# Kernel optimization log

Hardware: AMD Instinct MI355X
Metric: run time of the kernel (lower is better)

Reference implementation:

```python
import jax, jax.numpy as jnp
import numpy as np

N = 50000        # nodes
E = 800000       # edges (no self-loops; loops added in reference per PyG GATConv default)
IN = 128         # in_channels
OUT = 32         # out_channels
HEADS = 4
HID = HEADS * OUT  # 128
NEG_SLOPE = 0.2
BN_EPS = 1e-5
INV_SQRT2 = 0.7071067811865476


def setup_inputs() -> dict:
    key = jax.random.key(0)
    ks = jax.random.split(key, 20)
    x = jax.random.normal(ks[0], (N, IN), dtype=jnp.float32)
    src = jax.random.randint(ks[1], (E,), 0, N)
    dst = jax.random.randint(ks[2], (E,), 0, N)
    dst = jnp.where(src == dst, (dst + 1) % N, dst)  # no self-loops in base graph
    edge_index = jnp.stack([src, dst], axis=0)
    def lin(k, fan_in, shape):
        return jax.random.normal(k, shape, dtype=jnp.float32) / np.float32(np.sqrt(fan_in))
    return {
        "x": x,
        "edge_index": edge_index,
        "W1": lin(ks[3], IN, (IN, HID)),
        "att_src1": 0.1 * jax.random.normal(ks[4], (HEADS, OUT), dtype=jnp.float32),
        "att_dst1": 0.1 * jax.random.normal(ks[5], (HEADS, OUT), dtype=jnp.float32),
        "bias1": jnp.zeros((HID,), jnp.float32),
        "W2": lin(ks[6], HID, (HID, HID)),
        "att_src2": 0.1 * jax.random.normal(ks[7], (1, HID), dtype=jnp.float32),
        "att_dst2": 0.1 * jax.random.normal(ks[8], (1, HID), dtype=jnp.float32),
        "bias2": jnp.zeros((HID,), jnp.float32),
        "gamma1": jnp.ones((HID,), jnp.float32),
        "beta1": jnp.zeros((HID,), jnp.float32),
        "gamma2": jnp.ones((HID,), jnp.float32),
        "beta2": jnp.zeros((HID,), jnp.float32),
        "W_res": lin(ks[9], IN, (IN, HID)),
        "b_res": jnp.zeros((HID,), jnp.float32),
        "W_fin": lin(ks[10], HID, (HID, OUT)),
        "b_fin": jnp.zeros((OUT,), jnp.float32),
    }


def gat_conv(x, src, dst, W, a_src, a_dst, bias, heads, out_ch):
    h = (x @ W).reshape(-1, heads, out_ch)                    # [N, H, C]
    alpha_s = jnp.sum(h * a_src, axis=-1)                      # [N, H]
    alpha_d = jnp.sum(h * a_dst, axis=-1)                      # [N, H]
    e = jax.nn.leaky_relu(alpha_s[src] + alpha_d[dst], NEG_SLOPE)  # [E, H]
    # segment softmax over incoming edges of each destination node
    m = jax.ops.segment_max(e, dst, num_segments=N)
    e = jnp.exp(e - m[dst])
    denom = jax.ops.segment_sum(e, dst, num_segments=N)
    alpha = e / (denom[dst] + 1e-16)                           # [E, H]
    msg = h[src] * alpha[..., None]                            # [E, H, C]
    out = jax.ops.segment_sum(msg, dst, num_segments=N)        # [N, H, C]
    return out.reshape(-1, heads * out_ch) + bias


def batch_norm(h, gamma, beta):
    mu = h.mean(axis=0)
    var = jnp.mean((h - mu) ** 2, axis=0)  # biased, as torch BN training forward
    return (h - mu) * jax.lax.rsqrt(var + BN_EPS) * gamma + beta


def reference(x, edge_index, W1, att_src1, att_dst1, bias1, W2, att_src2, att_dst2,
              bias2, gamma1, beta1, gamma2, beta2, W_res, b_res, W_fin, b_fin):
    loops = jnp.arange(N, dtype=edge_index.dtype)
    src = jnp.concatenate([edge_index[0], loops])
    dst = jnp.concatenate([edge_index[1], loops])
    h = gat_conv(x, src, dst, W1, att_src1, att_dst1, bias1, HEADS, OUT)
    h = jax.nn.relu(batch_norm(h, gamma1, beta1))
    h = gat_conv(h, src, dst, W2, att_src2, att_dst2, bias2, 1, HID)
    h = jax.nn.relu(batch_norm(h, gamma2, beta2))
    residual = x @ W_res + b_res
    return ((h + residual) * INV_SQRT2) @ W_fin + b_fin        # [N, OUT]
```

## Files before the change

### kernel.cpp

```cpp
#include <hip/hip_runtime.h>
#include <hip/hip_fp16.h>
#include <type_traits>

#define NEG_SLOPE 0.2f
#define INV_SQRT2 0.7071067811865476f
#define BCAP 8192

typedef _Float16 half8 __attribute__((ext_vector_type(8)));
typedef float floatx4 __attribute__((ext_vector_type(4)));

__device__ __forceinline__ float lrelu(float x) { return x > 0.f ? x : NEG_SLOPE * x; }


__global__ __launch_bounds__(256) void prep_weights(const float* __restrict__ W1,
                                                    const float* __restrict__ W2,
                                                    const float* __restrict__ Wres,
                                                    const float* __restrict__ Wfin,
                                                    _Float16* __restrict__ W1t,
                                                    _Float16* __restrict__ W2t,
                                                    _Float16* __restrict__ Wrt,
                                                    _Float16* __restrict__ Wft,
                                                    int* __restrict__ bfill) {
    if (blockIdx.x == 0) bfill[threadIdx.x] = 0;
    int i = blockIdx.x * 256 + threadIdx.x;
    if (i < 16384) {
        int k = i >> 7, n = i & 127;
        W1t[n * 136 + k] = (_Float16)W1[i];
    } else if (i < 32768) {
        int j = i - 16384; int k = j >> 7, n = j & 127;
        W2t[n * 136 + k] = (_Float16)W2[j];
    } else if (i < 49152) {
        int j = i - 32768; int k = j >> 7, n = j & 127;
        Wrt[n * 136 + k] = (_Float16)Wres[j];
    } else if (i < 53248) {
        int j = i - 49152; int k = j >> 5, n = j & 31;
        Wft[n * 136 + k] = (_Float16)Wfin[j];
    }
}


__global__ __launch_bounds__(256) void bucket_scatter(const int* __restrict__ src,
                                                      const int* __restrict__ dst,
                                                      int* __restrict__ bucket_fill,
                                                      unsigned* __restrict__ staging,
                                                      int E, int N, int chunk) {
    __shared__ int lds[256];
    int tid = threadIdx.x;
    int M = E + N;
    int begin = blockIdx.x * chunk;
    int endc = min(begin + chunk, M);
    lds[tid] = 0;
    __syncthreads();
    for (int i = begin + tid; i < endc; i += 256) {
        int d = (i < E) ? dst[i] : (i - E);
        atomicAdd(&lds[d >> 8], 1);
    }
    __syncthreads();
    int h = lds[tid];
    int base = 0;
    if (h > 0) base = atomicAdd(&bucket_fill[tid], h);
    __syncthreads();
    lds[tid] = base;
    __syncthreads();
    for (int i = begin + tid; i < endc; i += 256) {
        int s, d;
        if (i < E) { s = src[i]; d = dst[i]; } else { s = d = i - E; }
        int b = d >> 8;
        int r = atomicAdd(&lds[b], 1);
        if (r < BCAP) staging[b * BCAP + r] = (unsigned)s | ((unsigned)(d & 255) << 24);
    }
}

__global__ __launch_bounds__(256) void fine_sort(const unsigned* __restrict__ staging,
                                                 const int* __restrict__ bucket_fill,
                                                 int* __restrict__ row_ptr,
                                                 int* __restrict__ csr_src, int NB, int N) {
    __shared__ int sb[256];
    __shared__ int c1[256];
    __shared__ int s1[256];
    int t = threadIdx.x;
    int b = blockIdx.x;
    int c = (t < NB) ? min(bucket_fill[t], BCAP) : 0;
    sb[t] = c;
    __syncthreads();
    for (int off = 1; off < 256; off <<= 1) {
        int add = (t >= off) ? sb[t - off] : 0;
        __syncthreads();
        sb[t] += add;
        __syncthreads();
    }
    int hi = sb[b];
    int lo = (b > 0) ? sb[b - 1] : 0;
    int cnt = hi - lo;
    if (b == NB - 1 && t == 0) row_ptr[N] = sb[NB - 1];
    const unsigned* stg = staging + (long)b * BCAP;
    c1[t] = 0;
    __syncthreads();
    for (int k = t; k < cnt; k += 256) atomicAdd(&c1[stg[k] >> 24], 1);
    __syncthreads();
    int v = c1[t];
    s1[t] = v;
    __syncthreads();
    for (int off = 1; off < 256; off <<= 1) {
        int add = (t >= off) ? s1[t - off] : 0;
        __syncthreads();
        s1[t] += add;
        __syncthreads();
    }
    int excl = s1[t] - v;
    int node = b * 256 + t;
    if (node < N) row_ptr[node] = lo + excl;
    c1[t] = lo + excl;
    __syncthreads();
    for (int k = t; k < cnt; k += 256) {
        unsigned e = stg[k];
        int p = atomicAdd(&c1[e >> 24], 1);
        csr_src[p] = (int)(e & 0xFFFFFFu);
    }
}


template <int NCOLS, bool DO_BN, int ATTN, typename AT>
__global__ __launch_bounds__(256) void mfma_gemm(const AT* __restrict__ A,
                                                 const _Float16* __restrict__ Wt,
                                                 const float* __restrict__ sc_,
                                                 const float* __restrict__ sh_,
                                                 const float* __restrict__ a_src,
                                                 const float* __restrict__ a_dst,
                                                 float* __restrict__ as_out,
                                                 float* __restrict__ ad_out,
                                                 _Float16* __restrict__ out_h,
                                                 int nrows) {
    __shared__ __align__(16) _Float16 Ws[NCOLS * 136];
    int tid = threadIdx.x;
    {
        const float4* srcp = (const float4*)Wt;
        float4* dstp = (float4*)Ws;
        for (int i = tid; i < NCOLS * 17; i += 256) dstp[i] = srcp[i];
    }
    __syncthreads();

    int wave = tid >> 6, lane = tid & 63;
    int lrow = lane & 15, quad = lane >> 4;
    int m0 = blockIdx.x * 128 + wave * 32;
    long r0 = min(m0 + lrow, nrows - 1);
    long r1 = min(m0 + 16 + lrow, nrows - 1);
    constexpr int NT = NCOLS / 16;
    floatx4 acc[2][NT];
#pragma unroll
    for (int ms = 0; ms < 2; ++ms)
#pragma unroll
        for (int nt = 0; nt < NT; ++nt) acc[ms][nt] = (floatx4){0.f, 0.f, 0.f, 0.f};

#pragma unroll
    for (int ks = 0; ks < 4; ++ks) {
        int k0 = ks * 32 + quad * 8;
        float av[2][8];
        if constexpr (std::is_same<AT, float>::value) {
            float4 f0 = *(const float4*)&A[r0 * 128 + k0];
            float4 f1 = *(const float4*)&A[r0 * 128 + k0 + 4];
            av[0][0] = f0.x; av[0][1] = f0.y; av[0][2] = f0.z; av[0][3] = f0.w;
            av[0][4] = f1.x; av[0][5] = f1.y; av[0][6] = f1.z; av[0][7] = f1.w;
            float4 g0 = *(const float4*)&A[r1 * 128 + k0];
            float4 g1 = *(const float4*)&A[r1 * 128 + k0 + 4];
            av[1][0] = g0.x; av[1][1] = g0.y; av[1][2] = g0.z; av[1][3] = g0.w;
            av[1][4] = g1.x; av[1][5] = g1.y; av[1][6] = g1.z; av[1][7] = g1.w;
        } else {
            half8 h0 = *(const half8*)&A[r0 * 128 + k0];
            half8 h1 = *(const half8*)&A[r1 * 128 + k0];
#pragma unroll
            for (int u = 0; u < 8; ++u) {
                av[0][u] = (float)h0[u];
                av[1][u] = (float)h1[u];
            }
        }
        if (DO_BN) {
            float4 sc0 = *(const float4*)&sc_[k0];
            float4 sc1 = *(const float4*)&sc_[k0 + 4];
            float4 sh0 = *(const float4*)&sh_[k0];
            float4 sh1 = *(const float4*)&sh_[k0 + 4];
            float scv[8] = {sc0.x, sc0.y, sc0.z, sc0.w, sc1.x, sc1.y, sc1.z, sc1.w};
            float shv[8] = {sh0.x, sh0.y, sh0.z, sh0.w, sh1.x, sh1.y, sh1.z, sh1.w};
#pragma unroll
            for (int ms = 0; ms < 2; ++ms)
#pragma unroll
                for (int u = 0; u < 8; ++u)
                    av[ms][u] = fmaxf(av[ms][u] * scv[u] + shv[u], 0.f);
        }
        half8 a0h, a1h;
#pragma unroll
        for (int u = 0; u < 8; ++u) {
            a0h[u] = (_Float16)av[0][u];
            a1h[u] = (_Float16)av[1][u];
        }
#pragma unroll
        for (int nt = 0; nt < NT; ++nt) {
            half8 b = *(half8*)&Ws[(nt * 16 + lrow) * 136 + k0];
            acc[0][nt] = __builtin_amdgcn_mfma_f32_16x16x32_f16(a0h, b, acc[0][nt], 0, 0, 0);
            acc[1][nt] = __builtin_amdgcn_mfma_f32_16x16x32_f16(a1h, b, acc[1][nt], 0, 0, 0);
        }
    }

#pragma unroll
    for (int ms = 0; ms < 2; ++ms) {
#pragma unroll
        for (int nt = 0; nt < NT; ++nt) {
            int col = nt * 16 + lrow;
#pragma unroll
            for (int reg = 0; reg < 4; ++reg) {
                int r = m0 + ms * 16 + quad * 4 + reg;
                if (r < nrows) out_h[(long)r * NCOLS + col] = (_Float16)acc[ms][nt][reg];
            }
        }
    }

    if constexpr (ATTN > 0) {
        float asrc_l[NT], adst_l[NT];
#pragma unroll
        for (int nt = 0; nt < NT; ++nt) {
            asrc_l[nt] = a_src[nt * 16 + lrow];
            adst_l[nt] = a_dst[nt * 16 + lrow];
        }
#pragma unroll
        for (int ms = 0; ms < 2; ++ms) {
#pragma unroll
            for (int reg = 0; reg < 4; ++reg) {
                int r = m0 + ms * 16 + quad * 4 + reg;
                if constexpr (ATTN == 4) {
                    float ps[4], pd[4];
#pragma unroll
                    for (int h = 0; h < 4; ++h) {
                        ps[h] = acc[ms][2 * h][reg] * asrc_l[2 * h] +
                                acc[ms][2 * h + 1][reg] * asrc_l[2 * h + 1];
                        pd[h] = acc[ms][2 * h][reg] * adst_l[2 * h] +
                                acc[ms][2 * h + 1][reg] * adst_l[2 * h + 1];
                    }
#pragma unroll
                    for (int off = 1; off < 16; off <<= 1) {
#pragma unroll
                        for (int h = 0; h < 4; ++h) {
                            ps[h] += __shfl_xor(ps[h], off);
                            pd[h] += __shfl_xor(pd[h], off);
                        }
                    }
                    if (r < nrows && lrow < 4) {
                        float psv = lrow == 0 ? ps[0] : lrow == 1 ? ps[1]
                                  : lrow == 2 ? ps[2] : ps[3];
                        float pdv = lrow == 0 ? pd[0] : lrow == 1 ? pd[1]
                                  : lrow == 2 ? pd[2] : pd[3];
                        as_out[r * 4 + lrow] = psv;
                        ad_out[r * 4 + lrow] = pdv;
                    }
                } else {
                    float ps = 0.f, pd = 0.f;
#pragma unroll
                    for (int nt = 0; nt < NT; ++nt) {
                        ps += acc[ms][nt][reg] * asrc_l[nt];
                        pd += acc[ms][nt][reg] * adst_l[nt];
                    }
#pragma unroll
                    for (int off = 1; off < 16; off <<= 1) {
                        ps += __shfl_xor(ps, off);
                        pd += __shfl_xor(pd, off);
                    }
                    if (r < nrows && lrow == 0) {
                        as_out[r] = ps;
                        ad_out[r] = pd;
                    }
                }
            }
        }
    }
}


__global__ __launch_bounds__(256) void final_fused(const float* __restrict__ x,
                                                   const _Float16* __restrict__ nb,
                                                   const _Float16* __restrict__ Wrt,
                                                   const _Float16* __restrict__ Wft,
                                                   const float* __restrict__ b_res,
                                                   const float* __restrict__ sc_,
                                                   const float* __restrict__ sh_,
                                                   const float* __restrict__ b_fin,
                                                   float* __restrict__ out, int nrows) {
    __shared__ __align__(16) _Float16 Wr[128 * 136];
    __shared__ __align__(16) _Float16 Wf[32 * 136];
    __shared__ __align__(16) _Float16 Rt[128 * 136];
    int tid = threadIdx.x;
    {
        const float4* srcp = (const float4*)Wrt;
        float4* dstp = (float4*)Wr;
        for (int i = tid; i < 128 * 17; i += 256) dstp[i] = srcp[i];
        const float4* srcf = (const float4*)Wft;
        float4* dstf = (float4*)Wf;
        for (int i = tid; i < 32 * 17; i += 256) dstf[i] = srcf[i];
    }
    __syncthreads();

    int wave = tid >> 6, lane = tid & 63;
    int lrow = lane & 15, quad = lane >> 4;
    int m0 = blockIdx.x * 128 + wave * 32;
    long r0 = min(m0 + lrow, nrows - 1);
    long r1 = min(m0 + 16 + lrow, nrows - 1);

    floatx4 acc[2][8];
#pragma unroll
    for (int ms = 0; ms < 2; ++ms)
#pragma unroll
        for (int nt = 0; nt < 8; ++nt) acc[ms][nt] = (floatx4){0.f, 0.f, 0.f, 0.f};
#pragma unroll
    for (int ks = 0; ks < 4; ++ks) {
        int k0 = ks * 32 + quad * 8;
        half8 a0h, a1h;
        {
            float4 f0 = *(const float4*)&x[r0 * 128 + k0];
            float4 f1 = *(const float4*)&x[r0 * 128 + k0 + 4];
            float4 g0 = *(const float4*)&x[r1 * 128 + k0];
            float4 g1 = *(const float4*)&x[r1 * 128 + k0 + 4];
            a0h[0] = (_Float16)f0.x; a0h[1] = (_Float16)f0.y;
            a0h[2] = (_Float16)f0.z; a0h[3] = (_Float16)f0.w;
            a0h[4] = (_Float16)f1.x; a0h[5] = (_Float16)f1.y;
            a0h[6] = (_Float16)f1.z; a0h[7] = (_Float16)f1.w;
            a1h[0] = (_Float16)g0.x; a1h[1] = (_Float16)g0.y;
            a1h[2] = (_Float16)g0.z; a1h[3] = (_Float16)g0.w;
            a1h[4] = (_Float16)g1.x; a1h[5] = (_Float16)g1.y;
            a1h[6] = (_Float16)g1.z; a1h[7] = (_Float16)g1.w;
        }
#pragma unroll
        for (int nt = 0; nt < 8; ++nt) {
            half8 b = *(half8*)&Wr[(nt * 16 + lrow) * 136 + k0];
            acc[0][nt] = __builtin_amdgcn_mfma_f32_16x16x32_f16(a0h, b, acc[0][nt], 0, 0, 0);
            acc[1][nt] = __builtin_amdgcn_mfma_f32_16x16x32_f16(a1h, b, acc[1][nt], 0, 0, 0);
        }
    }
#pragma unroll
    for (int ms = 0; ms < 2; ++ms) {
#pragma unroll
        for (int nt = 0; nt < 8; ++nt) {
            int col = nt * 16 + lrow;
            float bv = b_res[col];
#pragma unroll
            for (int reg = 0; reg < 4; ++reg) {
                int lr = wave * 32 + ms * 16 + quad * 4 + reg;
                Rt[lr * 136 + col] = (_Float16)(acc[ms][nt][reg] + bv);
            }
        }
    }
    __syncthreads();

    floatx4 fac[2][2];
#pragma unroll
    for (int ms = 0; ms < 2; ++ms)
#pragma unroll
        for (int nt = 0; nt < 2; ++nt) fac[ms][nt] = (floatx4){0.f, 0.f, 0.f, 0.f};
#pragma unroll
    for (int ks = 0; ks < 4; ++ks) {
        int k0 = ks * 32 + quad * 8;
        float4 sc0 = *(const float4*)&sc_[k0];
        float4 sc1 = *(const float4*)&sc_[k0 + 4];
        float4 sh0 = *(const float4*)&sh_[k0];
        float4 sh1 = *(const float4*)&sh_[k0 + 4];
        float scv[8] = {sc0.x, sc0.y, sc0.z, sc0.w, sc1.x, sc1.y, sc1.z, sc1.w};
        float shv[8] = {sh0.x, sh0.y, sh0.z, sh0.w, sh1.x, sh1.y, sh1.z, sh1.w};
        half8 n0 = *(const half8*)&nb[r0 * 128 + k0];
        half8 n1 = *(const half8*)&nb[r1 * 128 + k0];
        int lr0 = wave * 32 + lrow;
        int lr1 = wave * 32 + 16 + lrow;
        half8 e0 = *(const half8*)&Rt[lr0 * 136 + k0];
        half8 e1 = *(const half8*)&Rt[lr1 * 136 + k0];
        half8 a0h, a1h;
#pragma unroll
        for (int u = 0; u < 8; ++u) {
            float v0 = fmaxf((float)n0[u] * scv[u] + shv[u], 0.f);
            float v1 = fmaxf((float)n1[u] * scv[u] + shv[u], 0.f);
            a0h[u] = (_Float16)((v0 + (float)e0[u]) * INV_SQRT2);
            a1h[u] = (_Float16)((v1 + (float)e1[u]) * INV_SQRT2);
        }
#pragma unroll
        for (int nt = 0; nt < 2; ++nt) {
            half8 b = *(half8*)&Wf[(nt * 16 + lrow) * 136 + k0];
            fac[0][nt] = __builtin_amdgcn_mfma_f32_16x16x32_f16(a0h, b, fac[0][nt], 0, 0, 0);
            fac[1][nt] = __builtin_amdgcn_mfma_f32_16x16x32_f16(a1h, b, fac[1][nt], 0, 0, 0);
        }
    }
#pragma unroll
    for (int ms = 0; ms < 2; ++ms) {
#pragma unroll
        for (int nt = 0; nt < 2; ++nt) {
            int col = nt * 16 + lrow;
            float bv = b_fin[col];
#pragma unroll
            for (int reg = 0; reg < 4; ++reg) {
                int r = m0 + ms * 16 + quad * 4 + reg;
                if (r < nrows) out[(long)r * 32 + col] = fac[ms][nt][reg] + bv;
            }
        }
    }
}


__global__ __launch_bounds__(256) void gat_agg_h4(const _Float16* __restrict__ h,
                                                  const float* __restrict__ as,
                                                  const float* __restrict__ ad,
                                                  const int* __restrict__ row_ptr,
                                                  const int* __restrict__ csr_src,
                                                  const float* __restrict__ bias,
                                                  _Float16* __restrict__ out, int n) {
    long gt = blockIdx.x * (long)blockDim.x + threadIdx.x;
    int node = (int)(gt >> 6);
    if (node >= n) return;
    int lane = threadIdx.x & 63;
    int lg = lane & 15, g = lane >> 4;
    int hh = lg >> 2;
    int start = row_ptr[node], end = row_ptr[node + 1];
    float adh = ad[node * 4 + hh];
    float acc[8] = {0, 0, 0, 0, 0, 0, 0, 0};
    float t = 0.f;
    for (int j = start; j < end; j += 16) {
        int s[4];
        float av[4];
#pragma unroll
        for (int k = 0; k < 4; ++k) {
            int je = j + g + 4 * k;
            bool vk = je < end;
            int jc = vk ? je : start;
            s[k] = csr_src[jc];
            av[k] = vk ? 1.f : 0.f;
        }
        float asv[4];
#pragma unroll
        for (int k = 0; k < 4; ++k) asv[k] = as[s[k] * 4 + hh];
        half8 hv[4];
#pragma unroll
        for (int k = 0; k < 4; ++k) hv[k] = *(const half8*)&h[(long)s[k] * 128 + lg * 8];
#pragma unroll
        for (int k = 0; k < 4; ++k) {
            float a = av[k] * __expf(lrelu(asv[k] + adh));
            t += a;
#pragma unroll
            for (int u = 0; u < 8; ++u) acc[u] += (float)hv[k][u] * a;
        }
    }
#pragma unroll
    for (int off = 16; off < 64; off <<= 1) {
        t += __shfl_xor(t, off);
#pragma unroll
        for (int u = 0; u < 8; ++u) acc[u] += __shfl_xor(acc[u], off);
    }
    if (g == 0) {
        float inv = 1.f / (t + 1e-16f);
        int cb = lg * 8;
        float4 b0 = *(const float4*)&bias[cb];
        float4 b1 = *(const float4*)&bias[cb + 4];
        half8 o;
        o[0] = (_Float16)(acc[0] * inv + b0.x);
        o[1] = (_Float16)(acc[1] * inv + b0.y);
        o[2] = (_Float16)(acc[2] * inv + b0.z);
        o[3] = (_Float16)(acc[3] * inv + b0.w);
        o[4] = (_Float16)(acc[4] * inv + b1.x);
        o[5] = (_Float16)(acc[5] * inv + b1.y);
        o[6] = (_Float16)(acc[6] * inv + b1.z);
        o[7] = (_Float16)(acc[7] * inv + b1.w);
        *(half8*)&out[(long)node * 128 + cb] = o;
    }
}

__global__ __launch_bounds__(256) void gat_agg_h1(const _Float16* __restrict__ h,
                                                  const float* __restrict__ as,
                                                  const float* __restrict__ ad,
                                                  const int* __restrict__ row_ptr,
                                                  const int* __restrict__ csr_src,
                                                  const float* __restrict__ bias,
                                                  _Float16* __restrict__ out, int n) {
    long gt = blockIdx.x * (long)blockDim.x + threadIdx.x;
    int node = (int)(gt >> 6);
    if (node >= n) return;
    int lane = threadIdx.x & 63;
    int lg = lane & 15, g = lane >> 4;
    int start = row_ptr[node], end = row_ptr[node + 1];
    float adn = ad[node];
    float acc[8] = {0, 0, 0, 0, 0, 0, 0, 0};
    float t = 0.f;
    for (int j = start; j < end; j += 16) {
        int s[4];
        float av[4];
#pragma unroll
        for (int k = 0; k < 4; ++k) {
            int je = j + g + 4 * k;
            bool vk = je < end;
            int jc = vk ? je : start;
            s[k] = csr_src[jc];
            av[k] = vk ? 1.f : 0.f;
        }
        float asv[4];
#pragma unroll
        for (int k = 0; k < 4; ++k) asv[k] = as[s[k]];
        half8 hv[4];
#pragma unroll
        for (int k = 0; k < 4; ++k) hv[k] = *(const half8*)&h[(long)s[k] * 128 + lg * 8];
#pragma unroll
        for (int k = 0; k < 4; ++k) {
            float a = av[k] * __expf(lrelu(asv[k] + adn));
            t += a;
#pragma unroll
            for (int u = 0; u < 8; ++u) acc[u] += (float)hv[k][u] * a;
        }
    }
#pragma unroll
    for (int off = 16; off < 64; off <<= 1) {
        t += __shfl_xor(t, off);
#pragma unroll
        for (int u = 0; u < 8; ++u) acc[u] += __shfl_xor(acc[u], off);
    }
    if (g == 0) {
        float inv = 1.f / (t + 1e-16f);
        int cb = lg * 8;
        float4 b0 = *(const float4*)&bias[cb];
        float4 b1 = *(const float4*)&bias[cb + 4];
        half8 o;
        o[0] = (_Float16)(acc[0] * inv + b0.x);
        o[1] = (_Float16)(acc[1] * inv + b0.y);
        o[2] = (_Float16)(acc[2] * inv + b0.z);
        o[3] = (_Float16)(acc[3] * inv + b0.w);
        o[4] = (_Float16)(acc[4] * inv + b1.x);
        o[5] = (_Float16)(acc[5] * inv + b1.y);
        o[6] = (_Float16)(acc[6] * inv + b1.z);
        o[7] = (_Float16)(acc[7] * inv + b1.w);
        *(half8*)&out[(long)node * 128 + cb] = o;
    }
}


__global__ __launch_bounds__(256) void bn_part(const _Float16* __restrict__ h,
                                               float* __restrict__ partial, int n) {
    int tid = threadIdx.x;
    int lg = tid & 15;
    int rg = tid >> 4;
    int b = blockIdx.x;
    int chunk = (n + gridDim.x - 1) / (int)gridDim.x;
    int r0 = b * chunk;
    int r1 = min(r0 + chunk, n);
    float fs[8] = {0, 0, 0, 0, 0, 0, 0, 0};
    float fq[8] = {0, 0, 0, 0, 0, 0, 0, 0};
    for (int r = r0 + rg; r < r1; r += 16) {
        half8 hv = *(const half8*)&h[(long)r * 128 + lg * 8];
#pragma unroll
        for (int u = 0; u < 8; ++u) {
            float v = (float)hv[u];
            fs[u] += v;
            fq[u] += v * v;
        }
    }
#pragma unroll
    for (int off = 16; off < 64; off <<= 1) {
#pragma unroll
        for (int u = 0; u < 8; ++u) {
            fs[u] += __shfl_xor(fs[u], off);
            fq[u] += __shfl_xor(fq[u], off);
        }
    }
    __shared__ float reds[4][128], redq[4][128];
    int wave = tid >> 6, lane = tid & 63;
    if (lane < 16) {
#pragma unroll
        for (int u = 0; u < 8; ++u) {
            reds[wave][lane * 8 + u] = fs[u];
            redq[wave][lane * 8 + u] = fq[u];
        }
    }
    __syncthreads();
    if (tid < 128) {
        float s = reds[0][tid] + reds[1][tid] + reds[2][tid] + reds[3][tid];
        float q = redq[0][tid] + redq[1][tid] + redq[2][tid] + redq[3][tid];
        partial[b * 256 + tid] = s;
        partial[b * 256 + 128 + tid] = q;
    }
}

__global__ __launch_bounds__(1024) void bn_reduce(const float* __restrict__ partial,
                                                  const float* __restrict__ gamma,
                                                  const float* __restrict__ beta,
                                                  float* __restrict__ scale,
                                                  float* __restrict__ shift, float invN) {
    __shared__ float lds_s[8][128], lds_q[8][128];
    int c = threadIdx.x & 127;
    int sl = threadIdx.x >> 7;
    float s = 0.f, q = 0.f;
#pragma unroll 4
    for (int k = sl; k < 256; k += 8) {
        s += partial[k * 256 + c];
        q += partial[k * 256 + 128 + c];
    }
    lds_s[sl][c] = s;
    lds_q[sl][c] = q;
    __syncthreads();
    if (threadIdx.x < 128) {
        float S = 0.f, Q = 0.f;
#pragma unroll
        for (int i = 0; i < 8; ++i) { S += lds_s[i][c]; Q += lds_q[i][c]; }
        float mean = S * invN;
        float var = Q * invN - mean * mean;
        float sc = gamma[c] * rsqrtf(var + 1e-5f);
        scale[c] = sc;
        shift[c] = beta[c] - mean * sc;
    }
}


extern "C" void kernel_launch(void* const* d_in, const int* in_sizes, int n_in,
                              void* d_out, int out_size, void* d_ws, size_t ws_size,
                              hipStream_t stream) {
    const float* x        = (const float*)d_in[0];
    const int*   ei       = (const int*)d_in[1];
    const float* W1       = (const float*)d_in[2];
    const float* att_src1 = (const float*)d_in[3];
    const float* att_dst1 = (const float*)d_in[4];
    const float* bias1    = (const float*)d_in[5];
    const float* W2       = (const float*)d_in[6];
    const float* att_src2 = (const float*)d_in[7];
    const float* att_dst2 = (const float*)d_in[8];
    const float* bias2    = (const float*)d_in[9];
    const float* gamma1   = (const float*)d_in[10];
    const float* beta1    = (const float*)d_in[11];
    const float* gamma2   = (const float*)d_in[12];
    const float* beta2    = (const float*)d_in[13];
    const float* W_res    = (const float*)d_in[14];
    const float* b_res    = (const float*)d_in[15];
    const float* W_fin    = (const float*)d_in[16];
    const float* b_fin    = (const float*)d_in[17];
    float* out = (float*)d_out;

    const int N = in_sizes[0] / 128;
    const int E = in_sizes[1] / 2;
    const int M = E + N;
    const int NB = (N + 255) >> 8;
    const int* srcA = ei;
    const int* dstA = ei + E;

    char* w = (char*)d_ws;
    size_t off = 0;
    auto alloc = [&](size_t bytes) -> void* {
        off = (off + 255) & ~(size_t)255;
        void* p = w + off;
        off += bytes;
        return p;
    };
    __half*    hb      = (__half*)alloc((size_t)N * 128 * 2);
    _Float16*  nb      = (_Float16*)alloc((size_t)N * 128 * 2);
    unsigned*  staging = (unsigned*)alloc((size_t)NB * BCAP * 4);
    int*       csr     = (int*)alloc((size_t)M * 4);
    int*       row_ptr = (int*)alloc((size_t)(N + 1) * 4);
    int*       bfill   = (int*)alloc((size_t)256 * 4);
    float*     bnpart  = (float*)alloc((size_t)256 * 256 * 4);
    float*     as1     = (float*)alloc((size_t)N * 4 * 4);
    float*     ad1     = (float*)alloc((size_t)N * 4 * 4);
    float*     as2     = (float*)alloc((size_t)N * 4);
    float*     ad2     = (float*)alloc((size_t)N * 4);
    _Float16*  W1t     = (_Float16*)alloc((size_t)128 * 136 * 2);
    _Float16*  W2t     = (_Float16*)alloc((size_t)128 * 136 * 2);
    _Float16*  Wrt     = (_Float16*)alloc((size_t)128 * 136 * 2);
    _Float16*  Wft     = (_Float16*)alloc((size_t)32 * 136 * 2);
    float*     scale1  = (float*)alloc(128 * 4);
    float*     shift1  = (float*)alloc(128 * 4);
    float*     scale2  = (float*)alloc(128 * 4);
    float*     shift2  = (float*)alloc(128 * 4);

    const int grid_mfma  = (N + 127) / 128;
    const int grid_nodes = (N + 3) / 4;
    const int scat_blks  = 256;
    const int chunk      = (M + scat_blks - 1) / scat_blks;
    const float invN = 1.0f / (float)N;

    prep_weights<<<208, 256, 0, stream>>>(W1, W2, W_res, W_fin, W1t, W2t, Wrt, Wft, bfill);

    bucket_scatter<<<scat_blks, 256, 0, stream>>>(srcA, dstA, bfill, staging, E, N, chunk);
    fine_sort<<<NB, 256, 0, stream>>>(staging, bfill, row_ptr, csr, NB, N);

    mfma_gemm<128, false, 4, float><<<grid_mfma, 256, 0, stream>>>(
        x, W1t, nullptr, nullptr, att_src1, att_dst1, as1, ad1, (_Float16*)hb, N);
    gat_agg_h4<<<grid_nodes, 256, 0, stream>>>((const _Float16*)hb, as1, ad1, row_ptr, csr,
                                               bias1, nb, N);

    bn_part<<<256, 256, 0, stream>>>(nb, bnpart, N);
    bn_reduce<<<1, 1024, 0, stream>>>(bnpart, gamma1, beta1, scale1, shift1, invN);

    mfma_gemm<128, true, 1, _Float16><<<grid_mfma, 256, 0, stream>>>(
        nb, W2t, scale1, shift1, att_src2, att_dst2, as2, ad2, (_Float16*)hb, N);
    gat_agg_h1<<<grid_nodes, 256, 0, stream>>>((const _Float16*)hb, as2, ad2, row_ptr, csr,
                                               bias2, nb, N);

    bn_part<<<256, 256, 0, stream>>>(nb, bnpart, N);
    bn_reduce<<<1, 1024, 0, stream>>>(bnpart, gamma2, beta2, scale2, shift2, invN);

    final_fused<<<grid_mfma, 256, 0, stream>>>(x, nb, Wrt, Wft, b_res, scale2, shift2,
                                               b_fin, out, N);
}
```

Before: 262.1 us.

## Merge edge scatter with conv1 GEMM and fold BN reduction into consumers

Runs the edge bucket scatter and the first-layer GEMM in one launch by splitting blocks between the two roles, so they overlap. Drops the separate bn_reduce kernels: each GEMM/final block now sums the BN partials itself into shared memory. Cuts the bn_part grid to 32 blocks so that per-block reduction stays cheap. This trades a few launches and one serial single-block kernel for redundant per-block reduction work and lower parallelism in bn_part.

```diff
diff --git a/kernel.cpp b/kernel.cpp
--- a/kernel.cpp
+++ b/kernel.cpp
@@ -5,6 +5,7 @@
 #define NEG_SLOPE 0.2f
 #define INV_SQRT2 0.7071067811865476f
 #define BCAP 8192
+#define NPART 32
 
 typedef _Float16 half8 __attribute__((ext_vector_type(8)));
 typedef float floatx4 __attribute__((ext_vector_type(4)));
@@ -39,11 +40,9 @@
 }
 
 
-__global__ __launch_bounds__(256) void bucket_scatter(const int* __restrict__ src,
-                                                      const int* __restrict__ dst,
-                                                      int* __restrict__ bucket_fill,
-                                                      unsigned* __restrict__ staging,
-                                                      int E, int N, int chunk) {
+__device__ void scatter_body(const int* __restrict__ src, const int* __restrict__ dst,
+                             int* __restrict__ bucket_fill, unsigned* __restrict__ staging,
+                             int E, int N, int chunk) {
     __shared__ int lds[256];
     int tid = threadIdx.x;
     int M = E + N;
@@ -121,28 +120,39 @@
 
 
 template <int NCOLS, bool DO_BN, int ATTN, typename AT>
-__global__ __launch_bounds__(256) void mfma_gemm(const AT* __restrict__ A,
-                                                 const _Float16* __restrict__ Wt,
-                                                 const float* __restrict__ sc_,
-                                                 const float* __restrict__ sh_,
-                                                 const float* __restrict__ a_src,
-                                                 const float* __restrict__ a_dst,
-                                                 float* __restrict__ as_out,
-                                                 float* __restrict__ ad_out,
-                                                 _Float16* __restrict__ out_h,
-                                                 int nrows) {
+__device__ void gemm_body(int bid, const AT* __restrict__ A, const _Float16* __restrict__ Wt,
+                          const float* __restrict__ bnpart, const float* __restrict__ gamma,
+                          const float* __restrict__ beta, float invN,
+                          const float* __restrict__ a_src, const float* __restrict__ a_dst,
+                          float* __restrict__ as_out, float* __restrict__ ad_out,
+                          _Float16* __restrict__ out_h, int nrows) {
     __shared__ __align__(16) _Float16 Ws[NCOLS * 136];
+    __shared__ __align__(16) float bnsc[DO_BN ? 128 : 4];
+    __shared__ __align__(16) float bnsh[DO_BN ? 128 : 4];
     int tid = threadIdx.x;
     {
         const float4* srcp = (const float4*)Wt;
         float4* dstp = (float4*)Ws;
         for (int i = tid; i < NCOLS * 17; i += 256) dstp[i] = srcp[i];
     }
+    if (DO_BN && tid < 128) {
+        float s = 0.f, q = 0.f;
+#pragma unroll 8
+        for (int k = 0; k < NPART; ++k) {
+            s += bnpart[k * 256 + tid];
+            q += bnpart[k * 256 + 128 + tid];
+        }
+        float mean = s * invN;
+        float var = q * invN - mean * mean;
+        float sc = gamma[tid] * rsqrtf(var + 1e-5f);
+        bnsc[tid] = sc;
+        bnsh[tid] = beta[tid] - mean * sc;
+    }
     __syncthreads();
 
     int wave = tid >> 6, lane = tid & 63;
     int lrow = lane & 15, quad = lane >> 4;
-    int m0 = blockIdx.x * 128 + wave * 32;
+    int m0 = bid * 128 + wave * 32;
     long r0 = min(m0 + lrow, nrows - 1);
     long r1 = min(m0 + 16 + lrow, nrows - 1);
     constexpr int NT = NCOLS / 16;
@@ -175,10 +185,10 @@
             }
         }
         if (DO_BN) {
-            float4 sc0 = *(const float4*)&sc_[k0];
-            float4 sc1 = *(const float4*)&sc_[k0 + 4];
-            float4 sh0 = *(const float4*)&sh_[k0];
-            float4 sh1 = *(const float4*)&sh_[k0 + 4];
+            float4 sc0 = *(const float4*)&bnsc[k0];
+            float4 sc1 = *(const float4*)&bnsc[k0 + 4];
+            float4 sh0 = *(const float4*)&bnsh[k0];
+            float4 sh1 = *(const float4*)&bnsh[k0 + 4];
             float scv[8] = {sc0.x, sc0.y, sc0.z, sc0.w, sc1.x, sc1.y, sc1.z, sc1.w};
             float shv[8] = {sh0.x, sh0.y, sh0.z, sh0.w, sh1.x, sh1.y, sh1.z, sh1.w};
 #pragma unroll
@@ -274,18 +284,56 @@
 }
 
 
+__global__ __launch_bounds__(256) void scatter_conv1(const int* __restrict__ src,
+                                                     const int* __restrict__ dst,
+                                                     int* __restrict__ bucket_fill,
+                                                     unsigned* __restrict__ staging,
+                                                     int E, int Nn, int chunk, int scat_blks,
+                                                     const float* __restrict__ x,
+                                                     const _Float16* __restrict__ W1t,
+                                                     const float* __restrict__ a_src,
+                                                     const float* __restrict__ a_dst,
+                                                     float* __restrict__ as_out,
+                                                     float* __restrict__ ad_out,
+                                                     _Float16* __restrict__ out_h, int nrows) {
+    if ((int)blockIdx.x < scat_blks) {
+        scatter_body(src, dst, bucket_fill, staging, E, Nn, chunk);
+    } else {
+        gemm_body<128, false, 4, float>(blockIdx.x - scat_blks, x, W1t, nullptr, nullptr,
+                                        nullptr, 0.f, a_src, a_dst, as_out, ad_out, out_h,
+                                        nrows);
+    }
+}
+
+__global__ __launch_bounds__(256) void conv2_kernel(const _Float16* __restrict__ A,
+                                                    const _Float16* __restrict__ Wt,
+                                                    const float* __restrict__ bnpart,
+                                                    const float* __restrict__ gamma,
+                                                    const float* __restrict__ beta, float invN,
+                                                    const float* __restrict__ a_src,
+                                                    const float* __restrict__ a_dst,
+                                                    float* __restrict__ as_out,
+                                                    float* __restrict__ ad_out,
+                                                    _Float16* __restrict__ out_h, int nrows) {
+    gemm_body<128, true, 1, _Float16>(blockIdx.x, A, Wt, bnpart, gamma, beta, invN,
+                                      a_src, a_dst, as_out, ad_out, out_h, nrows);
+}
+
+
 __global__ __launch_bounds__(256) void final_fused(const float* __restrict__ x,
                                                    const _Float16* __restrict__ nb,
                                                    const _Float16* __restrict__ Wrt,
                                                    const _Float16* __restrict__ Wft,
                                                    const float* __restrict__ b_res,
-                                                   const float* __restrict__ sc_,
-                                                   const float* __restrict__ sh_,
+                                                   const float* __restrict__ bnpart,
+                                                   const float* __restrict__ gamma,
+                                                   const float* __restrict__ beta, float invN,
                                                    const float* __restrict__ b_fin,
                                                    float* __restrict__ out, int nrows) {
     __shared__ __align__(16) _Float16 Wr[128 * 136];
     __shared__ __align__(16) _Float16 Wf[32 * 136];
     __shared__ __align__(16) _Float16 Rt[128 * 136];
+    __shared__ __align__(16) float bnsc[128], bnsh[128];
     int tid = threadIdx.x;
     {
         const float4* srcp = (const float4*)Wrt;
@@ -294,6 +342,19 @@
         const float4* srcf = (const float4*)Wft;
         float4* dstf = (float4*)Wf;
         for (int i = tid; i < 32 * 17; i += 256) dstf[i] = srcf[i];
+    }
+    if (tid < 128) {
+        float s = 0.f, q = 0.f;
+#pragma unroll 8
+        for (int k = 0; k < NPART; ++k) {
+            s += bnpart[k * 256 + tid];
+            q += bnpart[k * 256 + 128 + tid];
+        }
+        float mean = s * invN;
+        float var = q * invN - mean * mean;
+        float sc = gamma[tid] * rsqrtf(var + 1e-5f);
+        bnsc[tid] = sc;
+        bnsh[tid] = beta[tid] - mean * sc;
     }
     __syncthreads();
 
@@ -356,10 +417,10 @@
 #pragma unroll
     for (int ks = 0; ks < 4; ++ks) {
         int k0 = ks * 32 + quad * 8;
-        float4 sc0 = *(const float4*)&sc_[k0];
-        float4 sc1 = *(const float4*)&sc_[k0 + 4];
-        float4 sh0 = *(const float4*)&sh_[k0];
-        float4 sh1 = *(const float4*)&sh_[k0 + 4];
+        float4 sc0 = *(const float4*)&bnsc[k0];
+        float4 sc1 = *(const float4*)&bnsc[k0 + 4];
+        float4 sh0 = *(const float4*)&bnsh[k0];
+        float4 sh1 = *(const float4*)&bnsh[k0 + 4];
         float scv[8] = {sc0.x, sc0.y, sc0.z, sc0.w, sc1.x, sc1.y, sc1.z, sc1.w};
         float shv[8] = {sh0.x, sh0.y, sh0.z, sh0.w, sh1.x, sh1.y, sh1.z, sh1.w};
         half8 n0 = *(const half8*)&nb[r0 * 128 + k0];
@@ -574,35 +635,6 @@
         float q = redq[0][tid] + redq[1][tid] + redq[2][tid] + redq[3][tid];
         partial[b * 256 + tid] = s;
         partial[b * 256 + 128 + tid] = q;
-    }
-}
-
-__global__ __launch_bounds__(1024) void bn_reduce(const float* __restrict__ partial,
-                                                  const float* __restrict__ gamma,
-                                                  const float* __restrict__ beta,
-                                                  float* __restrict__ scale,
-                                                  float* __restrict__ shift, float invN) {
-    __shared__ float lds_s[8][128], lds_q[8][128];
-    int c = threadIdx.x & 127;
-    int sl = threadIdx.x >> 7;
-    float s = 0.f, q = 0.f;
-#pragma unroll 4
-    for (int k = sl; k < 256; k += 8) {
-        s += partial[k * 256 + c];
-        q += partial[k * 256 + 128 + c];
-    }
-    lds_s[sl][c] = s;
-    lds_q[sl][c] = q;
-    __syncthreads();
-    if (threadIdx.x < 128) {
-        float S = 0.f, Q = 0.f;
-#pragma unroll
-        for (int i = 0; i < 8; ++i) { S += lds_s[i][c]; Q += lds_q[i][c]; }
-        float mean = S * invN;
-        float var = Q * invN - mean * mean;
-        float sc = gamma[c] * rsqrtf(var + 1e-5f);
-        scale[c] = sc;
-        shift[c] = beta[c] - mean * sc;
     }
 }
 
@@ -651,7 +683,7 @@
     int*       csr     = (int*)alloc((size_t)M * 4);
     int*       row_ptr = (int*)alloc((size_t)(N + 1) * 4);
     int*       bfill   = (int*)alloc((size_t)256 * 4);
-    float*     bnpart  = (float*)alloc((size_t)256 * 256 * 4);
+    float*     bnpart  = (float*)alloc((size_t)NPART * 256 * 4);
     float*     as1     = (float*)alloc((size_t)N * 4 * 4);
     float*     ad1     = (float*)alloc((size_t)N * 4 * 4);
     float*     as2     = (float*)alloc((size_t)N * 4);
@@ -660,10 +692,6 @@
     _Float16*  W2t     = (_Float16*)alloc((size_t)128 * 136 * 2);
     _Float16*  Wrt     = (_Float16*)alloc((size_t)128 * 136 * 2);
     _Float16*  Wft     = (_Float16*)alloc((size_t)32 * 136 * 2);
-    float*     scale1  = (float*)alloc(128 * 4);
-    float*     shift1  = (float*)alloc(128 * 4);
-    float*     scale2  = (float*)alloc(128 * 4);
-    float*     shift2  = (float*)alloc(128 * 4);
 
     const int grid_mfma  = (N + 127) / 128;
     const int grid_nodes = (N + 3) / 4;
@@ -673,25 +701,26 @@
 
     prep_weights<<<208, 256, 0, stream>>>(W1, W2, W_res, W_fin, W1t, W2t, Wrt, Wft, bfill);
 
-    bucket_scatter<<<scat_blks, 256, 0, stream>>>(srcA, dstA, bfill, staging, E, N, chunk);
+    scatter_conv1<<<scat_blks + grid_mfma, 256, 0, stream>>>(
+        srcA, dstA, bfill, staging, E, N, chunk, scat_blks,
+        x, W1t, att_src1, att_dst1, as1, ad1, (_Float16*)hb, N);
+
     fine_sort<<<NB, 256, 0, stream>>>(staging, bfill, row_ptr, csr, NB, N);
 
-    mfma_gemm<128, false, 4, float><<<grid_mfma, 256, 0, stream>>>(
-        x, W1t, nullptr, nullptr, att_src1, att_dst1, as1, ad1, (_Float16*)hb, N);
     gat_agg_h4<<<grid_nodes, 256, 0, stream>>>((const _Float16*)hb, as1, ad1, row_ptr, csr,
                                                bias1, nb, N);
 
-    bn_part<<<256, 256, 0, stream>>>(nb, bnpart, N);
-    bn_reduce<<<1, 1024, 0, stream>>>(bnpart, gamma1, beta1, scale1, shift1, invN);
-
-    mfma_gemm<128, true, 1, _Float16><<<grid_mfma, 256, 0, stream>>>(
-        nb, W2t, scale1, shift1, att_src2, att_dst2, as2, ad2, (_Float16*)hb, N);
+    bn_part<<<NPART, 256, 0, stream>>>(nb, bnpart, N);
+
+    conv2_kernel<<<grid_mfma, 256, 0, stream>>>(nb, W2t, bnpart, gamma1, beta1, invN,
+                                                att_src2, att_dst2, as2, ad2,
+                                                (_Float16*)hb, N);
+
     gat_agg_h1<<<grid_nodes, 256, 0, stream>>>((const _Float16*)hb, as2, ad2, row_ptr, csr,
                                                bias2, nb, N);
 
-    bn_part<<<256, 256, 0, stream>>>(nb, bnpart, N);
-    bn_reduce<<<1, 1024, 0, stream>>>(bnpart, gamma2, beta2, scale2, shift2, invN);
-
-    final_fused<<<grid_mfma, 256, 0, stream>>>(x, nb, Wrt, Wft, b_res, scale2, shift2,
-                                               b_fin, out, N);
-}
+    bn_part<<<NPART, 256, 0, stream>>>(nb, bnpart, N);
+
+    final_fused<<<grid_mfma, 256, 0, stream>>>(x, nb, Wrt, Wft, b_res, bnpart, gamma2, beta2,
+                                               invN, b_fin, out, N);
+}
```

Measured after the change: 303.8 us. 15.9% more time.
